# Kernel tuning notes

Hardware: AMD Instinct MI355X
Metric: run time of the kernel (lower is better)

The kernel has to match this reference:

```python
import jax, jax.numpy as jnp
import numpy as np

B, S, HID = 1, 2048, 2048
NH, NKV, D = 32, 8, 64
GROUPS = NH // NKV
THETA = 10000.0


def _rope_tables(seq_len, dim):
    inv_freq = 1.0 / (THETA ** (jnp.arange(0, dim, 2, dtype=jnp.float32) / dim))
    t = jnp.arange(seq_len, dtype=jnp.float32)
    freqs = jnp.outer(t, inv_freq)            # [S, D/2]
    emb = jnp.concatenate([freqs, freqs], axis=-1)  # [S, D]
    return jnp.cos(emb), jnp.sin(emb)


def _rotate_half(x):
    x1, x2 = jnp.split(x, 2, axis=-1)
    return jnp.concatenate([-x2, x1], axis=-1)


def setup_inputs() -> dict:
    key = jax.random.key(0)
    ks = jax.random.split(key, 8)
    hidden_states = jax.random.normal(ks[0], (B, S, HID), dtype=jnp.float32)
    # additive causal mask, 0 on/below diagonal, -1e9 above
    causal = jnp.tril(jnp.ones((S, S), dtype=bool))
    attention_mask = jnp.where(causal, 0.0, -1e9).astype(jnp.float32)[None, None]
    sc = 0.02
    Wq = sc * jax.random.normal(ks[1], (NH * D, HID), dtype=jnp.float32)
    bq = jnp.zeros((NH * D,), dtype=jnp.float32)
    Wk = sc * jax.random.normal(ks[2], (NKV * D, HID), dtype=jnp.float32)
    bk = jnp.zeros((NKV * D,), dtype=jnp.float32)
    Wv = sc * jax.random.normal(ks[3], (NKV * D, HID), dtype=jnp.float32)
    bv = jnp.zeros((NKV * D,), dtype=jnp.float32)
    Wo = sc * jax.random.normal(ks[4], (HID, NH * D), dtype=jnp.float32)
    return {"hidden_states": hidden_states, "attention_mask": attention_mask,
            "Wq": Wq, "bq": bq, "Wk": Wk, "bk": bk, "Wv": Wv, "bv": bv, "Wo": Wo}


def reference(hidden_states, attention_mask, Wq, bq, Wk, bk, Wv, bv, Wo):
    b, s, _ = hidden_states.shape
    q = (hidden_states @ Wq.T + bq).reshape(b, s, NH, D).transpose(0, 2, 1, 3)   # [B,NH,S,D]
    k = (hidden_states @ Wk.T + bk).reshape(b, s, NKV, D).transpose(0, 2, 1, 3)  # [B,NKV,S,D]
    v = (hidden_states @ Wv.T + bv).reshape(b, s, NKV, D).transpose(0, 2, 1, 3)
    cos, sin = _rope_tables(s, D)
    cos = cos[None, None]; sin = sin[None, None]
    q = q * cos + _rotate_half(q) * sin
    k = k * cos + _rotate_half(k) * sin
    # GQA: repeat KV heads to match query heads
    k = jnp.repeat(k, GROUPS, axis=1)  # [B,NH,S,D]
    v = jnp.repeat(v, GROUPS, axis=1)
    scores = jnp.einsum('bhqd,bhkd->bhqk', q, k) / jnp.sqrt(jnp.float32(D))
    scores = jnp.clip(scores, -50.0, 50.0)
    scores = scores + attention_mask
    probs = jax.nn.softmax(scores.astype(jnp.float32), axis=-1).astype(q.dtype)
    attn = jnp.einsum('bhqk,bhkd->bhqd', probs, v)
    attn = attn.transpose(0, 2, 1, 3).reshape(b, s, NH * D)
    return attn @ Wo.T
```

## Files before the change

kernel.cpp:

```cpp
#include <hip/hip_runtime.h>
#include <hip/hip_bf16.h>
#include <stdint.h>

typedef unsigned short u16;
typedef unsigned int u32;

#define S_LEN 2048
#define HID 2048
#define NH 32
#define NKV 8
#define HD 64
#define PIT 2080

using f32x4 = __attribute__((ext_vector_type(4))) float;
using bfrag = __attribute__((ext_vector_type(8))) short;

__device__ __forceinline__ float b2f(u16 u) {
  union { u32 i; float f; } c; c.i = ((u32)u) << 16; return c.f;
}
__device__ __forceinline__ u16 f2b(float f) {
  union { float f; u32 i; } c; c.f = f;
  u32 r = c.i + 0x7fffu + ((c.i >> 16) & 1u);
  return (u16)(r >> 16);
}
__device__ __forceinline__ uint4 cvt8(const float* __restrict__ p) {
  float4 a = *(const float4*)p;
  float4 b = *(const float4*)(p + 4);
  uint4 r;
  r.x = (u32)f2b(a.x) | ((u32)f2b(a.y) << 16);
  r.y = (u32)f2b(a.z) | ((u32)f2b(a.w) << 16);
  r.z = (u32)f2b(b.x) | ((u32)f2b(b.y) << 16);
  r.w = (u32)f2b(b.z) | ((u32)f2b(b.w) << 16);
  return r;
}

__device__ __forceinline__ void gl2lds16(const u16* g, u16* l) {
  __builtin_amdgcn_global_load_lds(
      (const __attribute__((address_space(1))) void*)g,
      (__attribute__((address_space(3))) void*)l,
      16, 0, 0);
}

__global__ void conv_f2b_p(const float* __restrict__ in, u16* __restrict__ out, int n8) {
  int i = blockIdx.x * 256 + threadIdx.x;
  if (i >= n8) return;
  int row = i >> 8;
  int col = (i & 255) * 8;
  *(uint4*)(out + (size_t)row * PIT + col) = cvt8(in + (size_t)row * 2048 + col);
}

__global__ __launch_bounds__(256, 3) void gemm_qkv(
    const u16* __restrict__ A, const u16* __restrict__ B,
    const float* __restrict__ bq, const float* __restrict__ bk, const float* __restrict__ bv,
    u16* __restrict__ Qb, u16* __restrict__ Kb, u16* __restrict__ Vt)
{
  __shared__ __align__(16) u16 As[64 * 32];
  __shared__ __align__(16) u16 Bs[128 * 32];
  __shared__ u16 strip_s[4][16 * 72];

  const int tid  = threadIdx.x;
  const int m0   = blockIdx.y * 64;
  const int n0   = blockIdx.x * 128;
  const int lane = tid & 63;
  const int w    = tid >> 6;
  const int wm   = w >> 1, wn = w & 1;
  const int quad = lane >> 4, l16 = lane & 15;

  const int srow = tid >> 2;
  const int scol = (tid & 3) * 8;
  const u16* ga = A + (size_t)(m0 + srow) * PIT + scol;
  const u16* gb = B + (size_t)(n0 + srow) * PIT + scol;
  u16* la = As + tid * 8;
  u16* lb = Bs + tid * 8;

  f32x4 zero = {0.f, 0.f, 0.f, 0.f};
  f32x4 acc[2][4];
#pragma unroll
  for (int mi = 0; mi < 2; ++mi)
#pragma unroll
    for (int ni = 0; ni < 4; ++ni) acc[mi][ni] = zero;

  for (int k0 = 0; k0 < HID; k0 += 32) {
    __syncthreads();
    gl2lds16(ga + k0, la);
    gl2lds16(gb + k0, lb);
    gl2lds16(gb + (size_t)64 * PIT + k0, lb + 2048);
    __syncthreads();

    bfrag af[2], bf[4];
#pragma unroll
    for (int i = 0; i < 2; ++i)
      af[i] = *(const bfrag*)&As[(wm * 32 + i * 16 + l16) * 32 + quad * 8];
#pragma unroll
    for (int i = 0; i < 4; ++i)
      bf[i] = *(const bfrag*)&Bs[(wn * 64 + i * 16 + l16) * 32 + quad * 8];
#pragma unroll
    for (int mi = 0; mi < 2; ++mi)
#pragma unroll
      for (int ni = 0; ni < 4; ++ni)
        acc[mi][ni] = __builtin_amdgcn_mfma_f32_16x16x32_bf16(af[mi], bf[ni], acc[mi][ni], 0, 0, 0);
  }

  u16* strip = strip_s[w];
  const int rr = lane >> 2;
  const int co = (lane & 3) * 8;

  if (n0 < 2048) {
#pragma unroll
    for (int mi = 0; mi < 2; ++mi) {
#pragma unroll
      for (int n01 = 0; n01 < 2; ++n01)
#pragma unroll
        for (int i = 0; i < 4; ++i) {
          int d  = n01 * 16 + l16;
          int c1 = n0 + wn * 64 + d;
          float x1 = acc[mi][n01][i]     + bq[c1];
          float x2 = acc[mi][n01 + 2][i] + bq[c1 + 32];
          float inv = exp2f(-(float)d * 0.41524101186092034f);
          float ang = (float)(m0 + wm * 32 + mi * 16 + quad * 4 + i) * inv;
          float cs = cosf(ang), sn = sinf(ang);
          strip[(quad * 4 + i) * 72 + d]      = f2b(x1 * cs - x2 * sn);
          strip[(quad * 4 + i) * 72 + d + 32] = f2b(x2 * cs + x1 * sn);
        }
      uint4 v0 = *(const uint4*)&strip[rr * 72 + co];
      uint4 v1 = *(const uint4*)&strip[rr * 72 + 32 + co];
      size_t gb2 = (size_t)(m0 + wm * 32 + mi * 16 + rr) * 2048 + n0 + wn * 64;
      *(uint4*)(Qb + gb2 + co)      = v0;
      *(uint4*)(Qb + gb2 + 32 + co) = v1;
    }
  } else if (n0 < 2560) {
    int cb = (n0 - 2048) + wn * 64;
#pragma unroll
    for (int mi = 0; mi < 2; ++mi) {
#pragma unroll
      for (int n01 = 0; n01 < 2; ++n01)
#pragma unroll
        for (int i = 0; i < 4; ++i) {
          int d  = n01 * 16 + l16;
          int cg = cb + d;
          float x1 = acc[mi][n01][i]     + bk[cg];
          float x2 = acc[mi][n01 + 2][i] + bk[cg + 32];
          float inv = exp2f(-(float)d * 0.41524101186092034f);
          float ang = (float)(m0 + wm * 32 + mi * 16 + quad * 4 + i) * inv;
          float cs = cosf(ang), sn = sinf(ang);
          strip[(quad * 4 + i) * 72 + d]      = f2b(x1 * cs - x2 * sn);
          strip[(quad * 4 + i) * 72 + d + 32] = f2b(x2 * cs + x1 * sn);
        }
      uint4 v0 = *(const uint4*)&strip[rr * 72 + co];
      uint4 v1 = *(const uint4*)&strip[rr * 72 + 32 + co];
      size_t gb2 = (size_t)(m0 + wm * 32 + mi * 16 + rr) * 512 + cb;
      *(uint4*)(Kb + gb2 + co)      = v0;
      *(uint4*)(Kb + gb2 + 32 + co) = v1;
    }
  } else {
    int cgb = (n0 - 2560) + wn * 64;
#pragma unroll
    for (int ni = 0; ni < 4; ++ni) {
      float bvv = bv[cgb + ni * 16 + l16];
#pragma unroll
      for (int mi = 0; mi < 2; ++mi)
#pragma unroll
        for (int i = 0; i < 4; ++i)
          strip[l16 * 72 + mi * 16 + quad * 4 + i] = f2b(acc[mi][ni][i] + bvv);
      uint4 v0 = *(const uint4*)&strip[rr * 72 + co];
      size_t gb2 = (size_t)(cgb + ni * 16 + rr) * PIT + m0 + wm * 32;
      *(uint4*)(Vt + gb2 + co) = v0;
    }
  }
}

__global__ __launch_bounds__(256, 3) void gemm_o(
    const u16* __restrict__ A, const u16* __restrict__ B, float* __restrict__ C)
{
  __shared__ __align__(16) u16 As[64 * 32];
  __shared__ __align__(16) u16 Bs[128 * 32];

  const int tid  = threadIdx.x;
  const int m0   = blockIdx.y * 64;
  const int n0   = blockIdx.x * 128;
  const int lane = tid & 63;
  const int w    = tid >> 6;
  const int wm   = w >> 1, wn = w & 1;
  const int quad = lane >> 4, l16 = lane & 15;

  const int srow = tid >> 2;
  const int scol = (tid & 3) * 8;
  const u16* ga = A + (size_t)(m0 + srow) * PIT + scol;
  const u16* gb = B + (size_t)(n0 + srow) * PIT + scol;
  u16* la = As + tid * 8;
  u16* lb = Bs + tid * 8;

  f32x4 zero = {0.f, 0.f, 0.f, 0.f};
  f32x4 acc[2][4];
#pragma unroll
  for (int mi = 0; mi < 2; ++mi)
#pragma unroll
    for (int ni = 0; ni < 4; ++ni) acc[mi][ni] = zero;

  for (int k0 = 0; k0 < HID; k0 += 32) {
    __syncthreads();
    gl2lds16(ga + k0, la);
    gl2lds16(gb + k0, lb);
    gl2lds16(gb + (size_t)64 * PIT + k0, lb + 2048);
    __syncthreads();

    bfrag af[2], bf[4];
#pragma unroll
    for (int i = 0; i < 2; ++i)
      af[i] = *(const bfrag*)&As[(wm * 32 + i * 16 + l16) * 32 + quad * 8];
#pragma unroll
    for (int i = 0; i < 4; ++i)
      bf[i] = *(const bfrag*)&Bs[(wn * 64 + i * 16 + l16) * 32 + quad * 8];
#pragma unroll
    for (int mi = 0; mi < 2; ++mi)
#pragma unroll
      for (int ni = 0; ni < 4; ++ni)
        acc[mi][ni] = __builtin_amdgcn_mfma_f32_16x16x32_bf16(af[mi], bf[ni], acc[mi][ni], 0, 0, 0);
  }

#pragma unroll
  for (int ni = 0; ni < 4; ++ni) {
    int col = n0 + wn * 64 + ni * 16 + l16;
#pragma unroll
    for (int mi = 0; mi < 2; ++mi)
#pragma unroll
      for (int i = 0; i < 4; ++i) {
        int row = m0 + wm * 32 + mi * 16 + quad * 4 + i;
        C[(size_t)row * 2048 + col] = acc[mi][ni][i];
      }
  }
}

__global__ __launch_bounds__(256) void attn_flash2(
    const u16* __restrict__ Qb, const u16* __restrict__ Kb,
    const u16* __restrict__ Vt, u16* __restrict__ Ab)
{
  __shared__ u16 Ps[4][2][16][72];

  const int h    = blockIdx.x;
  const int qbb  = 15 - (int)blockIdx.y;
  const int kvh  = h >> 2;
  const int tid  = threadIdx.x;
  const int lane = tid & 63;
  const int w    = tid >> 6;
  const int quad = lane >> 4, l16 = lane & 15;

  bfrag qf[2][2];
#pragma unroll
  for (int g = 0; g < 2; ++g) {
    const u16* qp = Qb + (size_t)(qbb * 128 + g * 64 + w * 16 + l16) * 2048 + h * 64 + quad * 8;
    qf[g][0] = *(const bfrag*)qp;
    qf[g][1] = *(const bfrag*)(qp + 32);
  }

  f32x4 zero = {0.f, 0.f, 0.f, 0.f};
  f32x4 o_acc[2][4];
  float lpart[2][4];
#pragma unroll
  for (int g = 0; g < 2; ++g)
#pragma unroll
    for (int nb = 0; nb < 4; ++nb) { o_acc[g][nb] = zero; lpart[g][nb] = 0.f; }

  const int kbmax = 2 * qbb + 1;
  for (int kb = 0; kb <= kbmax; ++kb) {
    bfrag kf0[4], kf1[4];
#pragma unroll
    for (int nb = 0; nb < 4; ++nb) {
      const u16* kp = Kb + (size_t)(kb * 64 + nb * 16 + l16) * 512 + kvh * 64 + quad * 8;
      kf0[nb] = *(const bfrag*)kp;
      kf1[nb] = *(const bfrag*)(kp + 32);
    }

#pragma unroll
    for (int g = 0; g < 2; ++g) {
      int t = 2 * qbb + g;
      if (kb > t) continue;
      f32x4 s_acc[4];
#pragma unroll
      for (int nb = 0; nb < 4; ++nb) {
        s_acc[nb] = __builtin_amdgcn_mfma_f32_16x16x32_bf16(qf[g][0], kf0[nb], zero, 0, 0, 0);
        s_acc[nb] = __builtin_amdgcn_mfma_f32_16x16x32_bf16(qf[g][1], kf1[nb], s_acc[nb], 0, 0, 0);
      }
      bool diag = (kb == t);
#pragma unroll
      for (int nb = 0; nb < 4; ++nb)
#pragma unroll
        for (int i = 0; i < 4; ++i) {
          float v = s_acc[nb][i] * 0.125f;
          v = fminf(50.0f, fmaxf(-50.0f, v));
          bool msk = diag && (nb * 16 + l16 > w * 16 + quad * 4 + i);
          float p = msk ? 0.0f : __expf(v);
          lpart[g][i] += p;
          Ps[w][g][quad * 4 + i][nb * 16 + l16] = f2b(p);
        }
    }

    bfrag vf0[4], vf1[4];
#pragma unroll
    for (int nb = 0; nb < 4; ++nb) {
      const u16* vp = Vt + (size_t)(kvh * 64 + nb * 16 + l16) * PIT + kb * 64 + quad * 8;
      vf0[nb] = *(const bfrag*)vp;
      vf1[nb] = *(const bfrag*)(vp + 32);
    }
#pragma unroll
    for (int g = 0; g < 2; ++g) {
      if (kb > 2 * qbb + g) continue;
      bfrag pf0 = *(const bfrag*)&Ps[w][g][l16][quad * 8];
      bfrag pf1 = *(const bfrag*)&Ps[w][g][l16][32 + quad * 8];
#pragma unroll
      for (int nb = 0; nb < 4; ++nb) {
        o_acc[g][nb] = __builtin_amdgcn_mfma_f32_16x16x32_bf16(pf0, vf0[nb], o_acc[g][nb], 0, 0, 0);
        o_acc[g][nb] = __builtin_amdgcn_mfma_f32_16x16x32_bf16(pf1, vf1[nb], o_acc[g][nb], 0, 0, 0);
      }
    }
  }

#pragma unroll
  for (int off = 1; off < 16; off <<= 1)
#pragma unroll
    for (int g = 0; g < 2; ++g)
#pragma unroll
      for (int i = 0; i < 4; ++i)
        lpart[g][i] += __shfl_xor(lpart[g][i], off, 64);

#pragma unroll
  for (int g = 0; g < 2; ++g)
#pragma unroll
    for (int i = 0; i < 4; ++i) {
      float inv = 1.0f / lpart[g][i];
      size_t rbase = (size_t)(qbb * 128 + g * 64 + w * 16 + quad * 4 + i) * PIT + h * 64;
#pragma unroll
      for (int nb = 0; nb < 4; ++nb)
        Ab[rbase + nb * 16 + l16] = f2b(o_acc[g][nb][i] * inv);
    }
}

extern "C" void kernel_launch(void* const* d_in, const int* in_sizes, int n_in,
                              void* d_out, int out_size, void* d_ws, size_t ws_size,
                              hipStream_t stream) {
  const float* hid = (const float*)d_in[0];
  const float* Wq = (const float*)d_in[2];
  const float* bq = (const float*)d_in[3];
  const float* Wk = (const float*)d_in[4];
  const float* bk = (const float*)d_in[5];
  const float* Wv = (const float*)d_in[6];
  const float* bv = (const float*)d_in[7];
  const float* Wo = (const float*)d_in[8];

  u16* hidb  = (u16*)d_ws;
  u16* Wqkvb = hidb + (size_t)2048 * PIT;
  u16* Qb    = Wqkvb + (size_t)3072 * PIT;
  u16* Kb    = Qb + 4194304;
  u16* Vt    = Kb + 1048576;
  u16* Wob   = hidb;
  u16* Ab    = Wqkvb;
  float* Ob  = (float*)d_out;

  conv_f2b_p<<<2048, 256, 0, stream>>>(hid, hidb, 524288);
  conv_f2b_p<<<2048, 256, 0, stream>>>(Wq, Wqkvb, 524288);
  conv_f2b_p<<<512, 256, 0, stream>>>(Wk, Wqkvb + (size_t)2048 * PIT, 131072);
  conv_f2b_p<<<512, 256, 0, stream>>>(Wv, Wqkvb + (size_t)2560 * PIT, 131072);

  gemm_qkv<<<dim3(24, 32), 256, 0, stream>>>(hidb, Wqkvb, bq, bk, bv, Qb, Kb, Vt);

  conv_f2b_p<<<2048, 256, 0, stream>>>(Wo, Wob, 524288);

  attn_flash2<<<dim3(32, 16), 256, 0, stream>>>(Qb, Kb, Vt, Ab);

  gemm_o<<<dim3(16, 32), 256, 0, stream>>>(Ab, Wob, Ob);
}
```

Measured before the change: 283.1 us.

## Double-buffer K/V fragments in attention, use exp2 softmax, fuse conversion launches

The attention loop is restructured to prefetch the next K/V tile into a second register set while computing the current one, with the diagonal blocks peeled out so the bulk loop carries no mask test. Softmax now uses exp2 with the scale folded into a log2e constant, and launch bounds request two blocks per CU. The four float-to-bf16 conversion launches for hidden states and Q/K/V weights are merged into one kernel. The double buffering raises register pressure, which could spill given the occupancy hint.

Measured after the change: 280.4 us. No clear change (-0.9%).

```diff
diff --git a/kernel.cpp b/kernel.cpp
--- a/kernel.cpp
+++ b/kernel.cpp
@@ -39,6 +39,19 @@
       (const __attribute__((address_space(1))) void*)g,
       (__attribute__((address_space(3))) void*)l,
       16, 0, 0);
+}
+
+__global__ void conv_all(const float* __restrict__ hid, const float* __restrict__ Wq,
+                         const float* __restrict__ Wk, const float* __restrict__ Wv,
+                         u16* __restrict__ hidb, u16* __restrict__ Wqkvb) {
+  int row = blockIdx.x;
+  int col = threadIdx.x * 8;
+  const float* src; u16* dst;
+  if (row < 2048)      { src = hid + (size_t)row * 2048;          dst = hidb  + (size_t)row * PIT; }
+  else if (row < 4096) { src = Wq + (size_t)(row - 2048) * 2048;  dst = Wqkvb + (size_t)(row - 2048) * PIT; }
+  else if (row < 4608) { src = Wk + (size_t)(row - 4096) * 2048;  dst = Wqkvb + (size_t)(row - 4096 + 2048) * PIT; }
+  else                 { src = Wv + (size_t)(row - 4608) * 2048;  dst = Wqkvb + (size_t)(row - 4608 + 2560) * PIT; }
+  *(uint4*)(dst + col) = cvt8(src + col);
 }
 
 __global__ void conv_f2b_p(const float* __restrict__ in, u16* __restrict__ out, int n8) {
@@ -231,7 +244,10 @@
   }
 }
 
-__global__ __launch_bounds__(256) void attn_flash2(
+#define SM_SC 0.18033688011112042f
+#define SM_UB 72.134752044448169f
+
+__global__ __launch_bounds__(256, 2) void attn_flash3(
     const u16* __restrict__ Qb, const u16* __restrict__ Kb,
     const u16* __restrict__ Vt, u16* __restrict__ Ab)
 {
@@ -253,6 +269,9 @@
     qf[g][1] = *(const bfrag*)(qp + 32);
   }
 
+  const u16* Kbase = Kb + (size_t)l16 * 512 + kvh * 64 + quad * 8;
+  const u16* Vbase = Vt + (size_t)(kvh * 64 + l16) * PIT + quad * 8;
+
   f32x4 zero = {0.f, 0.f, 0.f, 0.f};
   f32x4 o_acc[2][4];
   float lpart[2][4];
@@ -261,59 +280,100 @@
 #pragma unroll
     for (int nb = 0; nb < 4; ++nb) { o_acc[g][nb] = zero; lpart[g][nb] = 0.f; }
 
-  const int kbmax = 2 * qbb + 1;
-  for (int kb = 0; kb <= kbmax; ++kb) {
-    bfrag kf0[4], kf1[4];
-#pragma unroll
-    for (int nb = 0; nb < 4; ++nb) {
-      const u16* kp = Kb + (size_t)(kb * 64 + nb * 16 + l16) * 512 + kvh * 64 + quad * 8;
-      kf0[nb] = *(const bfrag*)kp;
-      kf1[nb] = *(const bfrag*)(kp + 32);
-    }
-
-#pragma unroll
-    for (int g = 0; g < 2; ++g) {
-      int t = 2 * qbb + g;
-      if (kb > t) continue;
-      f32x4 s_acc[4];
-#pragma unroll
-      for (int nb = 0; nb < 4; ++nb) {
-        s_acc[nb] = __builtin_amdgcn_mfma_f32_16x16x32_bf16(qf[g][0], kf0[nb], zero, 0, 0, 0);
-        s_acc[nb] = __builtin_amdgcn_mfma_f32_16x16x32_bf16(qf[g][1], kf1[nb], s_acc[nb], 0, 0, 0);
-      }
-      bool diag = (kb == t);
-#pragma unroll
-      for (int nb = 0; nb < 4; ++nb)
-#pragma unroll
-        for (int i = 0; i < 4; ++i) {
-          float v = s_acc[nb][i] * 0.125f;
-          v = fminf(50.0f, fmaxf(-50.0f, v));
-          bool msk = diag && (nb * 16 + l16 > w * 16 + quad * 4 + i);
-          float p = msk ? 0.0f : __expf(v);
-          lpart[g][i] += p;
-          Ps[w][g][quad * 4 + i][nb * 16 + l16] = f2b(p);
-        }
-    }
-
-    bfrag vf0[4], vf1[4];
-#pragma unroll
-    for (int nb = 0; nb < 4; ++nb) {
-      const u16* vp = Vt + (size_t)(kvh * 64 + nb * 16 + l16) * PIT + kb * 64 + quad * 8;
-      vf0[nb] = *(const bfrag*)vp;
-      vf1[nb] = *(const bfrag*)(vp + 32);
-    }
-#pragma unroll
-    for (int g = 0; g < 2; ++g) {
-      if (kb > 2 * qbb + g) continue;
-      bfrag pf0 = *(const bfrag*)&Ps[w][g][l16][quad * 8];
-      bfrag pf1 = *(const bfrag*)&Ps[w][g][l16][32 + quad * 8];
-#pragma unroll
-      for (int nb = 0; nb < 4; ++nb) {
-        o_acc[g][nb] = __builtin_amdgcn_mfma_f32_16x16x32_bf16(pf0, vf0[nb], o_acc[g][nb], 0, 0, 0);
-        o_acc[g][nb] = __builtin_amdgcn_mfma_f32_16x16x32_bf16(pf1, vf1[nb], o_acc[g][nb], 0, 0, 0);
-      }
-    }
-  }
+#define LOADKV(kb, k0, k1, v0, v1)                                              \
+  do {                                                                          \
+    _Pragma("unroll")                                                           \
+    for (int nb = 0; nb < 4; ++nb) {                                            \
+      const u16* kp = Kbase + (size_t)((kb) * 64 + nb * 16) * 512;              \
+      k0[nb] = *(const bfrag*)kp;                                               \
+      k1[nb] = *(const bfrag*)(kp + 32);                                        \
+      const u16* vp = Vbase + (size_t)(nb * 16) * PIT + (kb) * 64;              \
+      v0[nb] = *(const bfrag*)vp;                                               \
+      v1[nb] = *(const bfrag*)(vp + 32);                                        \
+    }                                                                           \
+  } while (0)
+
+#define QKT_SM_FULL(k0, k1, g)                                                  \
+  do {                                                                          \
+    f32x4 s_acc[4];                                                             \
+    _Pragma("unroll")                                                           \
+    for (int nb = 0; nb < 4; ++nb) {                                            \
+      s_acc[nb] = __builtin_amdgcn_mfma_f32_16x16x32_bf16(qf[g][0], k0[nb], zero, 0, 0, 0); \
+      s_acc[nb] = __builtin_amdgcn_mfma_f32_16x16x32_bf16(qf[g][1], k1[nb], s_acc[nb], 0, 0, 0); \
+    }                                                                           \
+    _Pragma("unroll")                                                           \
+    for (int nb = 0; nb < 4; ++nb)                                              \
+      _Pragma("unroll")                                                         \
+      for (int i = 0; i < 4; ++i) {                                             \
+        float u = s_acc[nb][i] * SM_SC;                                         \
+        u = fminf(SM_UB, fmaxf(-SM_UB, u));                                     \
+        float p = __builtin_amdgcn_exp2f(u);                                    \
+        lpart[g][i] += p;                                                       \
+        Ps[w][g][quad * 4 + i][nb * 16 + l16] = f2b(p);                         \
+      }                                                                         \
+  } while (0)
+
+#define QKT_SM_DIAG(k0, k1, g)                                                  \
+  do {                                                                          \
+    f32x4 s_acc[4];                                                             \
+    _Pragma("unroll")                                                           \
+    for (int nb = 0; nb < 4; ++nb) {                                            \
+      s_acc[nb] = __builtin_amdgcn_mfma_f32_16x16x32_bf16(qf[g][0], k0[nb], zero, 0, 0, 0); \
+      s_acc[nb] = __builtin_amdgcn_mfma_f32_16x16x32_bf16(qf[g][1], k1[nb], s_acc[nb], 0, 0, 0); \
+    }                                                                           \
+    _Pragma("unroll")                                                           \
+    for (int nb = 0; nb < 4; ++nb)                                              \
+      _Pragma("unroll")                                                         \
+      for (int i = 0; i < 4; ++i) {                                             \
+        float u = s_acc[nb][i] * SM_SC;                                         \
+        u = fminf(SM_UB, fmaxf(-SM_UB, u));                                     \
+        bool msk = (nb * 16 + l16 > w * 16 + quad * 4 + i);                     \
+        float p = msk ? 0.0f : __builtin_amdgcn_exp2f(u);                       \
+        lpart[g][i] += p;                                                       \
+        Ps[w][g][quad * 4 + i][nb * 16 + l16] = f2b(p);                         \
+      }                                                                         \
+  } while (0)
+
+#define PVACC(v0, v1, g)                                                        \
+  do {                                                                          \
+    bfrag pf0 = *(const bfrag*)&Ps[w][g][l16][quad * 8];                        \
+    bfrag pf1 = *(const bfrag*)&Ps[w][g][l16][32 + quad * 8];                   \
+    _Pragma("unroll")                                                           \
+    for (int nb = 0; nb < 4; ++nb) {                                            \
+      o_acc[g][nb] = __builtin_amdgcn_mfma_f32_16x16x32_bf16(pf0, v0[nb], o_acc[g][nb], 0, 0, 0); \
+      o_acc[g][nb] = __builtin_amdgcn_mfma_f32_16x16x32_bf16(pf1, v1[nb], o_acc[g][nb], 0, 0, 0); \
+    }                                                                           \
+  } while (0)
+
+  bfrag kX0[4], kX1[4], vX0[4], vX1[4];
+  bfrag kY0[4], kY1[4], vY0[4], vY1[4];
+
+  const int bulk  = 2 * qbb;
+  const int kbmax = bulk + 1;
+
+  LOADKV(0, kX0, kX1, vX0, vX1);
+
+  int kb = 0;
+  while (kb + 2 <= bulk) {
+    LOADKV(kb + 1, kY0, kY1, vY0, vY1);
+    QKT_SM_FULL(kX0, kX1, 0);
+    QKT_SM_FULL(kX0, kX1, 1);
+    PVACC(vX0, vX1, 0);
+    PVACC(vX0, vX1, 1);
+    LOADKV(kb + 2, kX0, kX1, vX0, vX1);
+    QKT_SM_FULL(kY0, kY1, 0);
+    QKT_SM_FULL(kY0, kY1, 1);
+    PVACC(vY0, vY1, 0);
+    PVACC(vY0, vY1, 1);
+    kb += 2;
+  }
+  LOADKV(kbmax, kY0, kY1, vY0, vY1);
+  QKT_SM_DIAG(kX0, kX1, 0);
+  QKT_SM_FULL(kX0, kX1, 1);
+  PVACC(vX0, vX1, 0);
+  PVACC(vX0, vX1, 1);
+  QKT_SM_DIAG(kY0, kY1, 1);
+  PVACC(vY0, vY1, 1);
 
 #pragma unroll
   for (int off = 1; off < 16; off <<= 1)
@@ -356,16 +416,13 @@
   u16* Ab    = Wqkvb;
   float* Ob  = (float*)d_out;
 
-  conv_f2b_p<<<2048, 256, 0, stream>>>(hid, hidb, 524288);
-  conv_f2b_p<<<2048, 256, 0, stream>>>(Wq, Wqkvb, 524288);
-  conv_f2b_p<<<512, 256, 0, stream>>>(Wk, Wqkvb + (size_t)2048 * PIT, 131072);
-  conv_f2b_p<<<512, 256, 0, stream>>>(Wv, Wqkvb + (size_t)2560 * PIT, 131072);
+  conv_all<<<5120, 256, 0, stream>>>(hid, Wq, Wk, Wv, hidb, Wqkvb);
 
   gemm_qkv<<<dim3(24, 32), 256, 0, stream>>>(hidb, Wqkvb, bq, bk, bv, Qb, Kb, Vt);
 
   conv_f2b_p<<<2048, 256, 0, stream>>>(Wo, Wob, 524288);
 
-  attn_flash2<<<dim3(32, 16), 256, 0, stream>>>(Qb, Kb, Vt, Ab);
+  attn_flash3<<<dim3(32, 16), 256, 0, stream>>>(Qb, Kb, Vt, Ab);
 
   gemm_o<<<dim3(16, 32), 256, 0, stream>>>(Ab, Wob, Ob);
 }
```
